# Kernel tuning notes

Hardware: AMD Instinct MI355X
Metric: run time of the kernel (lower is better)

Reference implementation:

```python
import jax, jax.numpy as jnp
import numpy as np

EPS = 1e-06
B, N, D, K, C = 16, 256, 4, 10, 100  # batch, nodes, pseudo dim, kernels, out_channels


def setup_inputs() -> dict:
    key = jax.random.key(0)
    k1, k2, k3, k4, k5, k6 = jax.random.split(key, 6)
    stdv = np.sqrt(6.0 / (K + D))
    x = jax.random.normal(k1, (B, N, K * C), dtype=jnp.float32)
    adj = (jax.random.uniform(k2, (B, N, N)) > 0.5).astype(jnp.float32)
    pseudo = jax.random.uniform(k3, (B, N, N, D), dtype=jnp.float32)
    mu = jax.random.uniform(k4, (K, D), minval=-stdv, maxval=stdv, dtype=jnp.float32)
    sigma = jax.random.uniform(k5, (K, D), minval=-stdv, maxval=stdv, dtype=jnp.float32)
    lim = 1.0 / np.sqrt(C)
    W = jax.random.uniform(k6, (C, C), minval=-lim, maxval=lim, dtype=jnp.float32)
    b = jnp.zeros((C,), dtype=jnp.float32)
    return {"x": x, "adj": adj, "pseudo": pseudo, "mu": mu, "sigma": sigma, "W": W, "b": b}


def reference(x, adj, pseudo, mu, sigma, W, b):
    # Gaussian kernel edge weights: [B,N,N,K]
    diff = pseudo[..., None, :] - mu            # [B,N,N,K,D]
    g = jnp.exp(jnp.sum(-0.5 * diff ** 2 / (EPS + sigma ** 2), axis=-1))
    ag = g * adj[..., None]                     # adjacency-masked weights [B,N,N,K]
    xk = x.reshape(B, N, K, C) @ W.T + b        # per-kernel linear  [B,N,K,C]
    # res[b,k,c,n] = sum_m ag[b,n,m,k] * xk[b,m,k,c]
    res = jnp.einsum('bnmk,bmkc->bkcn', ag, xk)
    return res.reshape(B, K * C, N)
```

## Files before the change

kernel.cpp:

```cpp
#include <hip/hip_runtime.h>

typedef __bf16 bf16;
typedef __attribute__((ext_vector_type(4)))  __bf16 bf16x4;
typedef __attribute__((ext_vector_type(8)))  __bf16 bf16x8;
typedef __attribute__((ext_vector_type(4)))  float  f32x4;
typedef __attribute__((ext_vector_type(16))) float  f32x16;

constexpr int B_ = 16, N_ = 256, K_ = 10, C_ = 100, CP_ = 112;
constexpr float NL2E = -0.7213475204444817f;
constexpr int BF_SLICE = 16 * 2 * 128 * 8;

__device__ inline bf16x8 cvt8(const float* p) {
    float4 a = *(const float4*)p, b = *(const float4*)(p + 4);
    bf16x8 r = {(bf16)a.x, (bf16)a.y, (bf16)a.z, (bf16)a.w,
                (bf16)b.x, (bf16)b.y, (bf16)b.z, (bf16)b.w};
    return r;
}
__device__ inline bf16x8 cvt4z(const float* p) {
    float4 a = *(const float4*)p;
    bf16x8 r = {(bf16)a.x, (bf16)a.y, (bf16)a.z, (bf16)a.w,
                (bf16)0.0f, (bf16)0.0f, (bf16)0.0f, (bf16)0.0f};
    return r;
}

__global__ __launch_bounds__(256, 2) void xk_gemm(
    const float* __restrict__ x, const float* __restrict__ W,
    const float* __restrict__ bias, bf16* __restrict__ xkT)
{
    __shared__ float xs[64 * 101 + 16];

    const int bid = blockIdx.x;
    const int xcd = bid & 7, s = bid >> 3;
    const int b  = xcd + 8 * (s / 40);
    const int rr = s % 40, kk = rr >> 2, mh = rr & 3;
    const int tid = threadIdx.x;
    const int w = tid >> 6, l = tid & 63, l31 = l & 31, h = l >> 5;
    const int c = w * 32 + l31;

    const float* xb = x + ((size_t)(b * N_ + mh * 64) * K_ + kk) * C_;
    #pragma unroll 2
    for (int idx = tid; idx < 1600; idx += 256) {
        int row = idx / 25, q = idx - row * 25;
        float4 v = *(const float4*)(xb + (size_t)row * (K_ * C_) + q * 4);
        *(float4*)(&xs[row * 101 + q * 4]) = v;
    }

    const bf16x8 zf = {(bf16)0.f,(bf16)0.f,(bf16)0.f,(bf16)0.f,
                       (bf16)0.f,(bf16)0.f,(bf16)0.f,(bf16)0.f};

    bf16x8 af[7];
    const float* Wrow = W + (size_t)c * C_;
    #pragma unroll
    for (int js = 0; js < 7; ++js) {
        const int jb = js * 16 + h * 8;
        af[js] = zf;
        if (c < C_) {
            if (jb + 8 <= C_)      af[js] = cvt8(Wrow + jb);
            else if (jb < C_)      af[js] = cvt4z(Wrow + jb);
        }
    }

    f32x16 acc0, acc1;
    #pragma unroll
    for (int r = 0; r < 16; ++r) {
        int crow = w * 32 + (r & 3) + 8 * (r >> 2) + 4 * h;
        float bv = (crow < C_) ? bias[crow] : 0.0f;
        acc0[r] = bv; acc1[r] = bv;
    }

    __syncthreads();

    #pragma unroll
    for (int js = 0; js < 7; ++js) {
        const int jb = js * 16 + h * 8;
        bf16x8 b0 = zf, b1 = zf;
        if (jb < C_) {
            b0 = cvt8(&xs[l31 * 101 + jb]);
            b1 = cvt8(&xs[(32 + l31) * 101 + jb]);
        }
        acc0 = __builtin_amdgcn_mfma_f32_32x32x16_bf16(af[js], b0, acc0, 0, 0, 0);
        acc1 = __builtin_amdgcn_mfma_f32_32x32x16_bf16(af[js], b1, acc1, 0, 0, 0);
    }

    bf16* op = xkT + (size_t)(b * K_ + kk) * BF_SLICE;
    const int m0g = mh * 64 + l31, m1g = m0g + 32;
    const int base0 = (((m0g >> 4) << 1) + ((m0g >> 3) & 1)) * 1024 + (m0g & 7);
    const int base1 = (((m1g >> 4) << 1) + ((m1g >> 3) & 1)) * 1024 + (m1g & 7);
    #pragma unroll
    for (int r = 0; r < 16; ++r) {
        const int crow = w * 32 + (r & 3) + 8 * (r >> 2) + 4 * h;
        op[base0 + crow * 8] = (bf16)acc0[r];
        op[base1 + crow * 8] = (bf16)acc1[r];
    }
}

__global__ __launch_bounds__(256, 2) void gauss_agg(
    const float* __restrict__ adj, const float* __restrict__ pseudo,
    const float* __restrict__ mu, const float* __restrict__ sigma,
    const bf16* __restrict__ xkT, float* __restrict__ out)
{
    __shared__ __align__(16) char lds[32 * 512];

    const int bid = blockIdx.x;
    const int xcd = bid & 7, s = bid >> 3;
    const int b  = xcd + 8 * (s / 80);
    const int rr = s % 80, kk = rr >> 3, nh = rr & 7;
    const int n32 = nh * 32;
    const int tid = threadIdx.x;

    float Av[4], Bv[4], ga = 0.0f;
    #pragma unroll
    for (int d = 0; d < 4; ++d) {
        float sg = sigma[kk * 4 + d];
        float al = NL2E / (1e-6f + sg * sg);
        float mv = mu[kk * 4 + d];
        Av[d] = al; Bv[d] = -2.0f * al * mv; ga += al * mv * mv;
    }

    const float* pbase = pseudo + (size_t)(b * N_ + n32) * N_ * 4;
    const float* abase = adj    + (size_t)(b * N_ + n32) * N_;
    #pragma unroll 4
    for (int i = 0; i < 8; ++i) {
        const int idx = i * 256 + tid;
        const int row = idx >> 6;
        const int m0  = (idx & 63) * 4;
        const float* pp = pbase + ((size_t)row * N_ + m0) * 4;
        float4 p0 = *(const float4*)(pp + 0);
        float4 p1 = *(const float4*)(pp + 4);
        float4 p2 = *(const float4*)(pp + 8);
        float4 p3 = *(const float4*)(pp + 12);
        float4 av = *(const float4*)(abase + (size_t)row * N_ + m0);

        float s0 = ga + Av[0]*p0.x*p0.x + Bv[0]*p0.x + Av[1]*p0.y*p0.y + Bv[1]*p0.y
                      + Av[2]*p0.z*p0.z + Bv[2]*p0.z + Av[3]*p0.w*p0.w + Bv[3]*p0.w;
        float s1 = ga + Av[0]*p1.x*p1.x + Bv[0]*p1.x + Av[1]*p1.y*p1.y + Bv[1]*p1.y
                      + Av[2]*p1.z*p1.z + Bv[2]*p1.z + Av[3]*p1.w*p1.w + Bv[3]*p1.w;
        float s2 = ga + Av[0]*p2.x*p2.x + Bv[0]*p2.x + Av[1]*p2.y*p2.y + Bv[1]*p2.y
                      + Av[2]*p2.z*p2.z + Bv[2]*p2.z + Av[3]*p2.w*p2.w + Bv[3]*p2.w;
        float s3 = ga + Av[0]*p3.x*p3.x + Bv[0]*p3.x + Av[1]*p3.y*p3.y + Bv[1]*p3.y
                      + Av[2]*p3.z*p3.z + Bv[2]*p3.z + Av[3]*p3.w*p3.w + Bv[3]*p3.w;

        bf16x4 o = {(bf16)(__builtin_amdgcn_exp2f(s0) * av.x),
                    (bf16)(__builtin_amdgcn_exp2f(s1) * av.y),
                    (bf16)(__builtin_amdgcn_exp2f(s2) * av.z),
                    (bf16)(__builtin_amdgcn_exp2f(s3) * av.w)};
        const int ch = m0 >> 3, half = (m0 >> 2) & 1;
        *(bf16x4*)(lds + row * 512 + ((ch ^ (row & 7)) * 16) + half * 8) = o;
    }
    __syncthreads();

    const int w = tid >> 6, l = tid & 63, l31 = l & 31, h = l >> 5;
    const bf16* bsl = xkT + (size_t)(b * K_ + kk) * BF_SLICE
                          + (size_t)(w * 32 + l31) * 8;
    f32x16 acc;
    #pragma unroll
    for (int i = 0; i < 16; ++i) acc[i] = 0.0f;

    #pragma unroll
    for (int ks = 0; ks < 16; ++ks) {
        bf16x8 af = *(const bf16x8*)(lds + l31 * 512 + (((ks * 2 + h) ^ (l31 & 7)) * 16));
        bf16x8 bf = *(const bf16x8*)(bsl + (size_t)(ks * 2 + h) * 1024);
        acc = __builtin_amdgcn_mfma_f32_32x32x16_bf16(af, bf, acc, 0, 0, 0);
    }

    const int c = w * 32 + l31;
    if (c < C_) {
        float* ob = out + (size_t)(b * K_ + kk) * C_ * N_ + (size_t)c * N_ + n32;
        #pragma unroll
        for (int q = 0; q < 4; ++q) {
            float4 v = {acc[4*q+0], acc[4*q+1], acc[4*q+2], acc[4*q+3]};
            *(float4*)(ob + 8 * q + 4 * h) = v;
        }
    }
}

extern "C" void kernel_launch(void* const* d_in, const int* in_sizes, int n_in,
                              void* d_out, int out_size, void* d_ws, size_t ws_size,
                              hipStream_t stream)
{
    const float* x      = (const float*)d_in[0];
    const float* adj    = (const float*)d_in[1];
    const float* pseudo = (const float*)d_in[2];
    const float* mu     = (const float*)d_in[3];
    const float* sigma  = (const float*)d_in[4];
    const float* W      = (const float*)d_in[5];
    const float* bias   = (const float*)d_in[6];
    float* out = (float*)d_out;
    bf16* xkT  = (bf16*)d_ws;

    hipLaunchKernelGGL(xk_gemm, dim3(640), dim3(256), 0, stream, x, W, bias, xkT);
    hipLaunchKernelGGL(gauss_agg, dim3(1280), dim3(256), 0, stream,
                       adj, pseudo, mu, sigma, xkT, out);
}
```

Measured before the change: 37.35 us.

## Fuse per-kernel linear GEMM into Gaussian aggregation kernel via LDS-resident xk

Merges the two launches into one kernel with one 512-thread block per (batch, kernel) pair. Each block computes the full 256-row xk slice into LDS, then loops over node tiles, building adjacency-masked Gaussian weights and running the MFMA aggregation. This removes the workspace round trip for xk and one launch. In exchange the grid shrinks from 1280 blocks to 160 with one block per CU, which cuts parallelism and serialises the phases inside each block.

```diff
diff --git a/kernel.cpp b/kernel.cpp
--- a/kernel.cpp
+++ b/kernel.cpp
@@ -6,9 +6,8 @@
 typedef __attribute__((ext_vector_type(4)))  float  f32x4;
 typedef __attribute__((ext_vector_type(16))) float  f32x16;
 
-constexpr int B_ = 16, N_ = 256, K_ = 10, C_ = 100, CP_ = 112;
+constexpr int B_ = 16, N_ = 256, K_ = 10, C_ = 100;
 constexpr float NL2E = -0.7213475204444817f;
-constexpr int BF_SLICE = 16 * 2 * 128 * 8;
 
 __device__ inline bf16x8 cvt8(const float* p) {
     float4 a = *(const float4*)p, b = *(const float4*)(p + 4);
@@ -23,27 +22,24 @@
     return r;
 }
 
-__global__ __launch_bounds__(256, 2) void xk_gemm(
-    const float* __restrict__ x, const float* __restrict__ W,
-    const float* __restrict__ bias, bf16* __restrict__ xkT)
+__global__ __launch_bounds__(512, 1) void fused_gauss(
+    const float* __restrict__ x, const float* __restrict__ adj,
+    const float* __restrict__ pseudo, const float* __restrict__ mu,
+    const float* __restrict__ sigma, const float* __restrict__ W,
+    const float* __restrict__ bias, float* __restrict__ out)
 {
     __shared__ float xs[64 * 101 + 16];
+    __shared__ bf16  xkt[32 * 128 * 8];
+    __shared__ __align__(16) char ag[2][32 * 512];
 
     const int bid = blockIdx.x;
-    const int xcd = bid & 7, s = bid >> 3;
-    const int b  = xcd + 8 * (s / 40);
-    const int rr = s % 40, kk = rr >> 2, mh = rr & 3;
+    const int xcd = bid & 7, slot = bid >> 3;
+    const int b  = xcd * 2 + slot / 10;
+    const int kk = slot % 10;
+
     const int tid = threadIdx.x;
     const int w = tid >> 6, l = tid & 63, l31 = l & 31, h = l >> 5;
-    const int c = w * 32 + l31;
-
-    const float* xb = x + ((size_t)(b * N_ + mh * 64) * K_ + kk) * C_;
-    #pragma unroll 2
-    for (int idx = tid; idx < 1600; idx += 256) {
-        int row = idx / 25, q = idx - row * 25;
-        float4 v = *(const float4*)(xb + (size_t)row * (K_ * C_) + q * 4);
-        *(float4*)(&xs[row * 101 + q * 4]) = v;
-    }
+    const int cw = w & 3, c = cw * 32 + l31;
 
     const bf16x8 zf = {(bf16)0.f,(bf16)0.f,(bf16)0.f,(bf16)0.f,
                        (bf16)0.f,(bf16)0.f,(bf16)0.f,(bf16)0.f};
@@ -59,54 +55,47 @@
             else if (jb < C_)      af[js] = cvt4z(Wrow + jb);
         }
     }
-
-    f32x16 acc0, acc1;
+    float bv_init[16];
     #pragma unroll
     for (int r = 0; r < 16; ++r) {
-        int crow = w * 32 + (r & 3) + 8 * (r >> 2) + 4 * h;
-        float bv = (crow < C_) ? bias[crow] : 0.0f;
-        acc0[r] = bv; acc1[r] = bv;
+        int crow = cw * 32 + (r & 3) + 8 * (r >> 2) + 4 * h;
+        bv_init[r] = (crow < C_) ? bias[crow] : 0.0f;
     }
 
-    __syncthreads();
+    const int mh2 = w >> 2;
+    #pragma unroll 1
+    for (int it = 0; it < 4; ++it) {
+        const float* xb = x + ((size_t)(b * N_ + it * 64) * K_ + kk) * C_;
+        #pragma unroll 1
+        for (int idx = tid; idx < 1600; idx += 512) {
+            int row = idx / 25, q = idx - row * 25;
+            float4 v = *(const float4*)(xb + (size_t)row * (K_ * C_) + q * 4);
+            *(float4*)(&xs[row * 101 + q * 4]) = v;
+        }
+        __syncthreads();
 
-    #pragma unroll
-    for (int js = 0; js < 7; ++js) {
-        const int jb = js * 16 + h * 8;
-        bf16x8 b0 = zf, b1 = zf;
-        if (jb < C_) {
-            b0 = cvt8(&xs[l31 * 101 + jb]);
-            b1 = cvt8(&xs[(32 + l31) * 101 + jb]);
+        f32x16 acc;
+        #pragma unroll
+        for (int r = 0; r < 16; ++r) acc[r] = bv_init[r];
+
+        const int mloc = mh2 * 32 + l31;
+        #pragma unroll
+        for (int js = 0; js < 7; ++js) {
+            const int jb = js * 16 + h * 8;
+            bf16x8 b0 = zf;
+            if (jb < C_) b0 = cvt8(&xs[mloc * 101 + jb]);
+            acc = __builtin_amdgcn_mfma_f32_32x32x16_bf16(af[js], b0, acc, 0, 0, 0);
         }
-        acc0 = __builtin_amdgcn_mfma_f32_32x32x16_bf16(af[js], b0, acc0, 0, 0, 0);
-        acc1 = __builtin_amdgcn_mfma_f32_32x32x16_bf16(af[js], b1, acc1, 0, 0, 0);
+
+        const int mg = it * 64 + mh2 * 32 + l31;
+        const int base = (((mg >> 4) << 1) + ((mg >> 3) & 1)) * 1024 + (mg & 7);
+        #pragma unroll
+        for (int r = 0; r < 16; ++r) {
+            const int crow = cw * 32 + (r & 3) + 8 * (r >> 2) + 4 * h;
+            xkt[base + crow * 8] = (bf16)acc[r];
+        }
+        __syncthreads();
     }
-
-    bf16* op = xkT + (size_t)(b * K_ + kk) * BF_SLICE;
-    const int m0g = mh * 64 + l31, m1g = m0g + 32;
-    const int base0 = (((m0g >> 4) << 1) + ((m0g >> 3) & 1)) * 1024 + (m0g & 7);
-    const int base1 = (((m1g >> 4) << 1) + ((m1g >> 3) & 1)) * 1024 + (m1g & 7);
-    #pragma unroll
-    for (int r = 0; r < 16; ++r) {
-        const int crow = w * 32 + (r & 3) + 8 * (r >> 2) + 4 * h;
-        op[base0 + crow * 8] = (bf16)acc0[r];
-        op[base1 + crow * 8] = (bf16)acc1[r];
-    }
-}
-
-__global__ __launch_bounds__(256, 2) void gauss_agg(
-    const float* __restrict__ adj, const float* __restrict__ pseudo,
-    const float* __restrict__ mu, const float* __restrict__ sigma,
-    const bf16* __restrict__ xkT, float* __restrict__ out)
-{
-    __shared__ __align__(16) char lds[32 * 512];
-
-    const int bid = blockIdx.x;
-    const int xcd = bid & 7, s = bid >> 3;
-    const int b  = xcd + 8 * (s / 80);
-    const int rr = s % 80, kk = rr >> 3, nh = rr & 7;
-    const int n32 = nh * 32;
-    const int tid = threadIdx.x;
 
     float Av[4], Bv[4], ga = 0.0f;
     #pragma unroll
@@ -117,60 +106,68 @@
         Av[d] = al; Bv[d] = -2.0f * al * mv; ga += al * mv * mv;
     }
 
-    const float* pbase = pseudo + (size_t)(b * N_ + n32) * N_ * 4;
-    const float* abase = adj    + (size_t)(b * N_ + n32) * N_;
-    #pragma unroll 4
-    for (int i = 0; i < 8; ++i) {
-        const int idx = i * 256 + tid;
-        const int row = idx >> 6;
-        const int m0  = (idx & 63) * 4;
-        const float* pp = pbase + ((size_t)row * N_ + m0) * 4;
-        float4 p0 = *(const float4*)(pp + 0);
-        float4 p1 = *(const float4*)(pp + 4);
-        float4 p2 = *(const float4*)(pp + 8);
-        float4 p3 = *(const float4*)(pp + 12);
-        float4 av = *(const float4*)(abase + (size_t)row * N_ + m0);
+    const int grp  = tid >> 8;
+    const int tid2 = tid & 255;
+    const int np   = w >> 2;
+    float* outb = out + (size_t)(b * K_ + kk) * C_ * N_;
 
-        float s0 = ga + Av[0]*p0.x*p0.x + Bv[0]*p0.x + Av[1]*p0.y*p0.y + Bv[1]*p0.y
-                      + Av[2]*p0.z*p0.z + Bv[2]*p0.z + Av[3]*p0.w*p0.w + Bv[3]*p0.w;
-        float s1 = ga + Av[0]*p1.x*p1.x + Bv[0]*p1.x + Av[1]*p1.y*p1.y + Bv[1]*p1.y
-                      + Av[2]*p1.z*p1.z + Bv[2]*p1.z + Av[3]*p1.w*p1.w + Bv[3]*p1.w;
-        float s2 = ga + Av[0]*p2.x*p2.x + Bv[0]*p2.x + Av[1]*p2.y*p2.y + Bv[1]*p2.y
-                      + Av[2]*p2.z*p2.z + Bv[2]*p2.z + Av[3]*p2.w*p2.w + Bv[3]*p2.w;
-        float s3 = ga + Av[0]*p3.x*p3.x + Bv[0]*p3.x + Av[1]*p3.y*p3.y + Bv[1]*p3.y
-                      + Av[2]*p3.z*p3.z + Bv[2]*p3.z + Av[3]*p3.w*p3.w + Bv[3]*p3.w;
+    #pragma unroll 1
+    for (int it = 0; it < 4; ++it) {
+        const int nh = it * 2 + grp;
+        const float* pbase = pseudo + (size_t)(b * N_ + nh * 32) * N_ * 4;
+        const float* abase = adj    + (size_t)(b * N_ + nh * 32) * N_;
+        char* agl = ag[grp];
+        #pragma unroll 4
+        for (int i = 0; i < 8; ++i) {
+            const int idx = i * 256 + tid2;
+            const int row = idx >> 6;
+            const int m0  = (idx & 63) * 4;
+            const float* pp = pbase + ((size_t)row * N_ + m0) * 4;
+            float4 p0 = *(const float4*)(pp + 0);
+            float4 p1 = *(const float4*)(pp + 4);
+            float4 p2 = *(const float4*)(pp + 8);
+            float4 p3 = *(const float4*)(pp + 12);
+            float4 av = *(const float4*)(abase + (size_t)row * N_ + m0);
 
-        bf16x4 o = {(bf16)(__builtin_amdgcn_exp2f(s0) * av.x),
-                    (bf16)(__builtin_amdgcn_exp2f(s1) * av.y),
-                    (bf16)(__builtin_amdgcn_exp2f(s2) * av.z),
-                    (bf16)(__builtin_amdgcn_exp2f(s3) * av.w)};
-        const int ch = m0 >> 3, half = (m0 >> 2) & 1;
-        *(bf16x4*)(lds + row * 512 + ((ch ^ (row & 7)) * 16) + half * 8) = o;
-    }
-    __syncthreads();
+            float s0 = ga + Av[0]*p0.x*p0.x + Bv[0]*p0.x + Av[1]*p0.y*p0.y + Bv[1]*p0.y
+                          + Av[2]*p0.z*p0.z + Bv[2]*p0.z + Av[3]*p0.w*p0.w + Bv[3]*p0.w;
+            float s1 = ga + Av[0]*p1.x*p1.x + Bv[0]*p1.x + Av[1]*p1.y*p1.y + Bv[1]*p1.y
+                          + Av[2]*p1.z*p1.z + Bv[2]*p1.z + Av[3]*p1.w*p1.w + Bv[3]*p1.w;
+            float s2 = ga + Av[0]*p2.x*p2.x + Bv[0]*p2.x + Av[1]*p2.y*p2.y + Bv[1]*p2.y
+                          + Av[2]*p2.z*p2.z + Bv[2]*p2.z + Av[3]*p2.w*p2.w + Bv[3]*p2.w;
+            float s3 = ga + Av[0]*p3.x*p3.x + Bv[0]*p3.x + Av[1]*p3.y*p3.y + Bv[1]*p3.y
+                          + Av[2]*p3.z*p3.z + Bv[2]*p3.z + Av[3]*p3.w*p3.w + Bv[3]*p3.w;
 
-    const int w = tid >> 6, l = tid & 63, l31 = l & 31, h = l >> 5;
-    const bf16* bsl = xkT + (size_t)(b * K_ + kk) * BF_SLICE
-                          + (size_t)(w * 32 + l31) * 8;
-    f32x16 acc;
-    #pragma unroll
-    for (int i = 0; i < 16; ++i) acc[i] = 0.0f;
+            bf16x4 o = {(bf16)(__builtin_amdgcn_exp2f(s0) * av.x),
+                        (bf16)(__builtin_amdgcn_exp2f(s1) * av.y),
+                        (bf16)(__builtin_amdgcn_exp2f(s2) * av.z),
+                        (bf16)(__builtin_amdgcn_exp2f(s3) * av.w)};
+            const int ch = m0 >> 3, half = (m0 >> 2) & 1;
+            *(bf16x4*)(agl + row * 512 + ((ch ^ (row & 7)) * 16) + half * 8) = o;
+        }
+        __syncthreads();
 
-    #pragma unroll
-    for (int ks = 0; ks < 16; ++ks) {
-        bf16x8 af = *(const bf16x8*)(lds + l31 * 512 + (((ks * 2 + h) ^ (l31 & 7)) * 16));
-        bf16x8 bf = *(const bf16x8*)(bsl + (size_t)(ks * 2 + h) * 1024);
-        acc = __builtin_amdgcn_mfma_f32_32x32x16_bf16(af, bf, acc, 0, 0, 0);
-    }
+        const char* agr = ag[np];
+        f32x16 acc;
+        #pragma unroll
+        for (int i = 0; i < 16; ++i) acc[i] = 0.0f;
 
-    const int c = w * 32 + l31;
-    if (c < C_) {
-        float* ob = out + (size_t)(b * K_ + kk) * C_ * N_ + (size_t)c * N_ + n32;
         #pragma unroll
-        for (int q = 0; q < 4; ++q) {
-            float4 v = {acc[4*q+0], acc[4*q+1], acc[4*q+2], acc[4*q+3]};
-            *(float4*)(ob + 8 * q + 4 * h) = v;
+        for (int ks = 0; ks < 16; ++ks) {
+            bf16x8 a8 = *(const bf16x8*)(agr + l31 * 512 + (((ks * 2 + h) ^ (l31 & 7)) * 16));
+            bf16x8 b8 = *(const bf16x8*)(&xkt[(ks * 2 + h) * 1024 + c * 8]);
+            acc = __builtin_amdgcn_mfma_f32_32x32x16_bf16(a8, b8, acc, 0, 0, 0);
         }
+
+        if (c < C_) {
+            float* ob = outb + (size_t)c * N_ + (it * 2 + np) * 32;
+            #pragma unroll
+            for (int q = 0; q < 4; ++q) {
+                float4 v = {acc[4*q+0], acc[4*q+1], acc[4*q+2], acc[4*q+3]};
+                *(float4*)(ob + 8 * q + 4 * h) = v;
+            }
+        }
+        __syncthreads();
     }
 }
 
@@ -186,9 +183,7 @@
     const float* W      = (const float*)d_in[5];
     const float* bias   = (const float*)d_in[6];
     float* out = (float*)d_out;
-    bf16* xkT  = (bf16*)d_ws;
 
-    hipLaunchKernelGGL(xk_gemm, dim3(640), dim3(256), 0, stream, x, W, bias, xkT);
-    hipLaunchKernelGGL(gauss_agg, dim3(1280), dim3(256), 0, stream,
-                       adj, pseudo, mu, sigma, xkT, out);
+    hipLaunchKernelGGL(fused_gauss, dim3(B_ * K_), dim3(512), 0, stream,
+                       x, adj, pseudo, mu, sigma, W, bias, out);
 }
```

After: 51.74 us. 1.39x slower.
